# Kernel optimization log

Hardware: AMD Instinct MI355X
Metric: run time of the kernel (lower is better)

## Reference

```python
import jax, jax.numpy as jnp
import numpy as np

D_MODEL = 1024
NUM_HEADS = 16
D_K = D_MODEL // NUM_HEADS
LN_EPS = 1e-5
NEG = -1e9


def setup_inputs() -> dict:
    key = jax.random.key(0)
    ks = jax.random.split(key, 12)
    B, S, D = 8, 1024, D_MODEL
    lim = 1.0 / np.sqrt(D)
    def lin(k):
        k1, k2 = jax.random.split(k)
        W = jax.random.uniform(k1, (D, D), jnp.float32, -lim, lim)
        b = jax.random.uniform(k2, (D,), jnp.float32, -lim, lim)
        return W, b
    Wq, bq = lin(ks[0])
    Wk, bk = lin(ks[1])
    Wv, bv = lin(ks[2])
    Wo, bo = lin(ks[3])
    return {
        "history_items": jax.random.normal(ks[4], (B, S, D), jnp.float32),
        "sequence_mask": jax.random.randint(ks[5], (B, S), 0, 2, jnp.int32),
        "Wq": Wq, "bq": bq, "Wk": Wk, "bk": bk,
        "Wv": Wv, "bv": bv, "Wo": Wo, "bo": bo,
        "ln_gamma": jnp.ones((D,), jnp.float32),
        "ln_beta": jnp.zeros((D,), jnp.float32),
    }


def reference(history_items, sequence_mask, Wq, bq, Wk, bk, Wv, bv, Wo, bo, ln_gamma, ln_beta):
    B, S, D = history_items.shape
    H, dk = NUM_HEADS, D_K
    # projections -> [B, H, S, dk]
    def proj(W, b):
        return (history_items @ W.T + b).reshape(B, S, H, dk).transpose(0, 2, 1, 3)
    q = proj(Wq, bq)
    k = proj(Wk, bk)
    v = proj(Wv, bv)
    # combined mask: causal [1,1,S,S] AND key-padding [B,1,1,S]
    causal = jnp.tril(jnp.ones((S, S), bool))[None, None]
    mask = jnp.logical_and(causal, (sequence_mask != 0)[:, None, None, :])
    scores = jnp.einsum('bhqd,bhkd->bhqk', q, k) / np.sqrt(dk).astype(np.float32)
    scores = jnp.where(mask, scores, NEG)
    attn = jax.nn.softmax(scores, axis=-1)
    ctx = jnp.einsum('bhqk,bhkd->bhqd', attn, v)  # [B,H,S,dk]
    concat = ctx.transpose(0, 2, 1, 3).reshape(B, S, D)
    out = concat @ Wo.T + bo
    x = out + history_items
    mu = jnp.mean(x, axis=-1, keepdims=True)
    var = jnp.mean((x - mu) ** 2, axis=-1, keepdims=True)
    return (x - mu) * jax.lax.rsqrt(var + LN_EPS) * ln_gamma + ln_beta
```

## Files before the change

### kernel.cpp

```cpp
#include <hip/hip_runtime.h>
#include <hip/hip_bf16.h>

#define B_ 8
#define S_ 1024
#define D_ 1024
#define H_ 16
#define DK_ 64
#define M_ (B_*S_)

#define QSCALE 0.1803368801111904f

typedef __attribute__((ext_vector_type(4))) float f32x4;
typedef __attribute__((ext_vector_type(8))) short bf16x8;
typedef __attribute__((ext_vector_type(4))) short s16x4;
typedef __hip_bfloat16 bf16;
typedef unsigned long long ull;

#define GLOAD_LDS16(gp, lp) __builtin_amdgcn_global_load_lds( \
    (const __attribute__((address_space(1))) void*)(gp), \
    (__attribute__((address_space(3))) void*)(lp), 16, 0, 0)

#define SBAR()   asm volatile("s_barrier" ::: "memory")
#define VMCNT(n) asm volatile("s_waitcnt vmcnt(" #n ")" ::: "memory")

__device__ __forceinline__ bf16x8 ld8(const bf16* p){ return *(const bf16x8*)p; }

__device__ __forceinline__ short bf16bits(float f){
  bf16 h = __float2bfloat16(f);
  return __builtin_bit_cast(short, h);
}
__device__ __forceinline__ float tof(short b){
  unsigned u = ((unsigned)(unsigned short)b) << 16;
  return __builtin_bit_cast(float, u);
}
__device__ __forceinline__ int cvtpk(float a, float b){
  int r; asm("v_cvt_pk_bf16_f32 %0, %1, %2" : "=v"(r) : "v"(a), "v"(b)); return r;
}

__device__ __forceinline__ bf16x8 ld8swz(const bf16* base, int row, int colb){
  int sw = colb ^ ((row & 7) << 4);
  return *(const bf16x8*)((const char*)base + row*128 + sw);
}

__global__ __launch_bounds__(256) void cast_all(const float* __restrict__ X,
    const float* __restrict__ w0, const float* __restrict__ w1,
    const float* __restrict__ w2, const float* __restrict__ w3,
    bf16* __restrict__ Xout, bf16* __restrict__ Wout){
  int bid = blockIdx.x;
  if (bid < 4096){
    int i = (bid*256 + threadIdx.x)*8;
    f32x4 a = *(const f32x4*)(X+i);
    f32x4 b = *(const f32x4*)(X+i+4);
    bf16x8 o;
    #pragma unroll
    for (int c=0;c<4;c++){ o[c] = bf16bits(a[c]); o[c+4] = bf16bits(b[c]); }
    *(bf16x8*)(Xout+i) = o;
  } else {
    int bb = bid - 4096;
    int sel = bb >> 9;
    const float* src = (sel==0)?w0:((sel==1)?w1:((sel==2)?w2:w3));
    int i = (((bb & 511)*256) + threadIdx.x)*8;
    f32x4 a = *(const f32x4*)(src+i);
    f32x4 b = *(const f32x4*)(src+i+4);
    bf16x8 o;
    #pragma unroll
    for (int c=0;c<4;c++){ o[c] = bf16bits(a[c]); o[c+4] = bf16bits(b[c]); }
    *(bf16x8*)(Wout + ((size_t)sel<<20) + i) = o;
  }
}

__global__ __launch_bounds__(256) void vmean_kernel(const bf16* __restrict__ Vt_g,
                                                    float* __restrict__ vmean){
  int r = blockIdx.x*4 + (threadIdx.x>>6);
  int lane = threadIdx.x & 63;
  const bf16* p = Vt_g + (((size_t)r)<<10) + lane*16;
  bf16x8 a = ld8(p), c = ld8(p+8);
  float s = 0.f;
  #pragma unroll
  for (int e=0;e<8;e++) s += tof(a[e]) + tof(c[e]);
  #pragma unroll
  for (int off=1;off<64;off<<=1) s += __shfl_xor(s, off);
  if (lane==0) vmean[r] = s * (1.f/1024.f);
}

template<int MODE>
__global__ __launch_bounds__(256) void gemm128(
    const bf16* __restrict__ A,
    const bf16* __restrict__ W0, const bf16* __restrict__ W1, const bf16* __restrict__ W2,
    const float* __restrict__ b0, const float* __restrict__ b1, const float* __restrict__ b2,
    bf16* __restrict__ o0, bf16* __restrict__ o1, bf16* __restrict__ o2,
    const float* __restrict__ resid, float* __restrict__ xout)
{
  const bf16* Wsel = W0; const float* bsel = b0;
  if (MODE==0){
    int z = blockIdx.z;
    Wsel = (z==0)?W0:((z==1)?W1:W2);
    bsel = (z==0)?b0:((z==1)?b1:b2);
  }
  __shared__ bf16 smem[4*128*64];
  const int tid = threadIdx.x, wid = tid>>6, lane = tid&63;
  const int lr = lane&15, lg = lane>>4;
  const int m0 = blockIdx.x*128, n0 = blockIdx.y*128;
  const int wr = wid>>1, wc = wid&1;
  f32x4 acc[4][4] = {};

  auto STAGE = [&](int k0, int bsel_){
    #pragma unroll
    for (int c=0;c<4;c++){
      int ldsoff = ((c<<2)|wid)<<10;
      int off = ldsoff + (lane<<4);
      int row = off>>7;
      int colb = (off&127) ^ ((row&7)<<4);
      GLOAD_LDS16(A   + (((size_t)(m0+row))<<10) + k0 + (colb>>1), (char*)smem + bsel_*32768 + ldsoff);
      GLOAD_LDS16(Wsel+ (((size_t)(n0+row))<<10) + k0 + (colb>>1), (char*)smem + bsel_*32768 + 16384 + ldsoff);
    }
  };

  STAGE(0, 0);
  int cur = 0;
  for (int kt=0; kt<16; kt++){
    if (kt < 15){ STAGE((kt+1)<<6, cur^1); VMCNT(8); }
    else        { VMCNT(0); }
    SBAR();
    __builtin_amdgcn_sched_barrier(0);
    const bf16* Asb = smem + cur*16384;
    const bf16* Bsb = Asb + 8192;
    bf16x8 af[4][2], bfv[4][2];
    #pragma unroll
    for (int m=0;m<4;m++){
      int row = wr*64 + m*16 + lr;
      af[m][0] = ld8swz(Asb, row, lg*16);
      af[m][1] = ld8swz(Asb, row, lg*16 + 64);
    }
    #pragma unroll
    for (int n=0;n<4;n++){
      int row = wc*64 + n*16 + lr;
      bfv[n][0] = ld8swz(Bsb, row, lg*16);
      bfv[n][1] = ld8swz(Bsb, row, lg*16 + 64);
    }
    #pragma unroll
    for (int m=0;m<4;m++)
      #pragma unroll
      for (int n=0;n<4;n++){
        acc[m][n] = __builtin_amdgcn_mfma_f32_16x16x32_bf16(af[m][0], bfv[n][0], acc[m][n],0,0,0);
        acc[m][n] = __builtin_amdgcn_mfma_f32_16x16x32_bf16(af[m][1], bfv[n][1], acc[m][n],0,0,0);
      }
    __builtin_amdgcn_sched_barrier(0);
    SBAR();
    cur ^= 1;
  }

  if (MODE==0){
    if (blockIdx.z == 2){
      __syncthreads();
      #pragma unroll
      for (int n=0;n<4;n++){
        int c = wc*64 + n*16 + lr;
        float bias = bsel[n0 + c];
        #pragma unroll
        for (int m=0;m<4;m++){
          int r0 = wr*64 + m*16 + lg*4;
          s16x4 pk;
          #pragma unroll
          for (int j=0;j<4;j++) pk[j] = bf16bits(acc[m][n][j] + bias);
          *(s16x4*)((char*)smem + c*256 + ((r0*2) ^ ((c&7)<<4))) = pk;
        }
      }
      __syncthreads();
      #pragma unroll
      for (int q=0;q<8;q++){
        int idx = tid + q*256;
        int c = idx>>4, r8 = idx&15;
        bf16x8 vv = *(const bf16x8*)((char*)smem + c*256 + ((r8*16) ^ ((c&7)<<4)));
        int col = n0 + c;  int h = col>>6, dd = col&63;
        int row0 = m0 + r8*8;  int bb = row0>>10, s0 = row0&1023;
        int a = (s0>>3)&3;
        int O = 16*(a&1) + 4*(a>>1);
        bf16* dst = o2 + ((((size_t)bb*H_ + h)*DK_ + dd)<<10) + (s0 & ~31) + O;
        s16x4 lo, hi;
        lo[0]=vv[0]; lo[1]=vv[1]; lo[2]=vv[2]; lo[3]=vv[3];
        hi[0]=vv[4]; hi[1]=vv[5]; hi[2]=vv[6]; hi[3]=vv[7];
        *(s16x4*)dst       = lo;
        *(s16x4*)(dst + 8) = hi;
      }
    } else {
      bf16* osel = (blockIdx.z==0) ? o0 : o1;
      const float qs = (blockIdx.z==0) ? QSCALE : 1.0f;
      #pragma unroll
      for (int n=0;n<4;n++){
        int col = n0 + wc*64 + n*16 + lr;
        float bias = bsel[col];
        int h = col>>6, dd = col&63;
        #pragma unroll
        for (int m=0;m<4;m++)
          #pragma unroll
          for (int j=0;j<4;j++){
            int row = m0 + wr*64 + m*16 + lg*4 + j;
            int bb = row>>10, s = row&1023;
            osel[((((size_t)bb*H_ + h)<<10) + s)*DK_ + dd] = __float2bfloat16((acc[m][n][j] + bias)*qs);
          }
      }
    }
  } else {
    #pragma unroll
    for (int n=0;n<4;n++){
      int col = n0 + wc*64 + n*16 + lr;
      float bias = bsel[col];
      #pragma unroll
      for (int m=0;m<4;m++)
        #pragma unroll
        for (int j=0;j<4;j++){
          int row = m0 + wr*64 + m*16 + lg*4 + j;
          size_t idx = (((size_t)row)<<10) + col;
          xout[idx] = acc[m][n][j] + bias + resid[idx];
        }
    }
  }
}

__global__ __launch_bounds__(512) void attn_kernel(
    const bf16* __restrict__ Q, const bf16* __restrict__ K, const bf16* __restrict__ Vt_g,
    const int* __restrict__ seqm, const float* __restrict__ vmean, bf16* __restrict__ ctxout)
{
  __shared__ bf16 Ks[2][64*64];
  __shared__ bf16 Vs[2][64*64];
  __shared__ int msk[1024];
  const int tid = threadIdx.x, wid = tid>>6, lane = tid&63;
  const int lr = lane&15, lg = lane>>4;
  const int bh = blockIdx.x, xb = blockIdx.y;
  const int b = bh>>4, h = bh&15;
  const bf16* Qb  = Q    + (size_t)bh * S_ * DK_;
  const bf16* Kb  = K    + (size_t)bh * S_ * DK_;
  const bf16* Vtb = Vt_g + (size_t)bh * DK_ * S_;
  for (int i=tid;i<1024;i+=512) msk[i] = seqm[b*1024+i];

  const int g0 = 8*xb + wid;
  const int rb0 = g0*16;
  const int rb1 = (63 - g0)*16;
  bf16x8 qf[2][2];
  {
    const bf16* p0 = Qb + (size_t)(rb0+lr)*DK_ + lg*8;
    const bf16* p1 = Qb + (size_t)(rb1+lr)*DK_ + lg*8;
    qf[0][0] = ld8(p0); qf[0][1] = ld8(p0+32);
    qf[1][0] = ld8(p1); qf[1][1] = ld8(p1+32);
  }
  f32x4 cacc[2][4] = {};
  float lsum[2] = {0.f, 0.f};

  auto STAGE = [&](int t, int bsel){
    const int j0 = t*64;
    int off = (wid<<10) + (lane<<4);
    int row = off>>7;
    int colb = (off&127) ^ ((row&7)<<4);
    GLOAD_LDS16(Kb  + (size_t)(j0+row)*DK_ + (colb>>1), (char*)&Ks[bsel][0] + (wid<<10));
    GLOAD_LDS16(Vtb + (((size_t)row)<<10) + j0 + (colb>>1), (char*)&Vs[bsel][0] + (wid<<10));
  };

  STAGE(0, 0);
  __syncthreads();

  const int bnt = ((1023 - 128*xb) >> 6) + 1;

  int cur = 0;
  for (int t=0; t<bnt; t++){
    VMCNT(0);
    SBAR();
    if (t+1 < bnt) STAGE(t+1, cur^1);
    const int j0 = t*64;
    if (j0 <= rb1 + 15){
      const bool act0 = (j0 <= rb0 + 15);
      ull bt = __ballot(msk[j0 + lane] != 0);
      unsigned btl = (unsigned)bt, bth = (unsigned)(bt >> 32);

      bf16x8 kf[4][2];
      #pragma unroll
      for (int nf=0;nf<4;nf++){
        kf[nf][0] = ld8swz(&Ks[cur][0], nf*16+lr, lg*16);
        kf[nf][1] = ld8swz(&Ks[cur][0], nf*16+lr, lg*16 + 64);
      }

      bf16x8 pf[2][2];
      #pragma unroll
      for (int mf=0;mf<2;mf++){
        if (mf==0 && !act0) continue;
        const int rbm = mf ? rb1 : rb0;
        const bool diag = (j0 + 63 > rbm);
        const int qrel = rbm + lr - j0;
        f32x4 sc[4] = {};
        __builtin_amdgcn_s_setprio(1);
        #pragma unroll
        for (int nf=0;nf<4;nf++){
          sc[nf] = __builtin_amdgcn_mfma_f32_16x16x32_bf16(kf[nf][0], qf[mf][0], sc[nf],0,0,0);
          sc[nf] = __builtin_amdgcn_mfma_f32_16x16x32_bf16(kf[nf][1], qf[mf][1], sc[nf],0,0,0);
        }
        __builtin_amdgcn_s_setprio(0);
        float ls = 0.f;
        #pragma unroll
        for (int nf=0;nf<4;nf++){
          unsigned hb2 = (nf<2) ? btl : bth;
          #pragma unroll
          for (int j=0;j<4;j++){
            float p = exp2f(sc[nf][j]);
            bool ok = ((hb2 >> (16*(nf&1) + 4*lg + j)) & 1u) != 0u;
            if (diag) ok = ok && (16*nf + 4*lg + j <= qrel);
            p = ok ? p : 0.f;
            sc[nf][j] = p;
            ls += p;
          }
        }
        lsum[mf] += ls;
        int4 w0, w1;
        w0.x = cvtpk(sc[0][0], sc[0][1]); w0.y = cvtpk(sc[0][2], sc[0][3]);
        w0.z = cvtpk(sc[1][0], sc[1][1]); w0.w = cvtpk(sc[1][2], sc[1][3]);
        w1.x = cvtpk(sc[2][0], sc[2][1]); w1.y = cvtpk(sc[2][2], sc[2][3]);
        w1.z = cvtpk(sc[3][0], sc[3][1]); w1.w = cvtpk(sc[3][2], sc[3][3]);
        pf[mf][0] = __builtin_bit_cast(bf16x8, w0);
        pf[mf][1] = __builtin_bit_cast(bf16x8, w1);
      }
      __builtin_amdgcn_s_setprio(1);
      #pragma unroll
      for (int df=0;df<4;df++){
        bf16x8 vf0 = ld8swz(&Vs[cur][0], df*16+lr, lg*16);
        bf16x8 vf1 = ld8swz(&Vs[cur][0], df*16+lr, lg*16 + 64);
        if (act0){
          cacc[0][df] = __builtin_amdgcn_mfma_f32_16x16x32_bf16(pf[0][0], vf0, cacc[0][df],0,0,0);
          cacc[0][df] = __builtin_amdgcn_mfma_f32_16x16x32_bf16(pf[0][1], vf1, cacc[0][df],0,0,0);
        }
        cacc[1][df] = __builtin_amdgcn_mfma_f32_16x16x32_bf16(pf[1][0], vf0, cacc[1][df],0,0,0);
        cacc[1][df] = __builtin_amdgcn_mfma_f32_16x16x32_bf16(pf[1][1], vf1, cacc[1][df],0,0,0);
      }
      __builtin_amdgcn_s_setprio(0);
    }
    cur ^= 1;
  }

  #pragma unroll
  for (int mf=0;mf<2;mf++){
    const int rbm = mf ? rb1 : rb0;
    float T = lsum[mf];
    T += __shfl_xor(T, 16);
    T += __shfl_xor(T, 32);
    float lden[4];
    #pragma unroll
    for (int j=0;j<4;j++)
      lden[j] = __shfl(T, (lane & 48) | (lg*4 + j));
    #pragma unroll
    for (int df=0;df<4;df++)
      #pragma unroll
      for (int j=0;j<4;j++){
        int srow = rbm + lg*4 + j;
        int dd = df*16 + lr;
        float v = cacc[mf][df][j] / lden[j];
        if (lden[j] < 1e-30f) v = vmean[bh*64 + dd];
        ctxout[((size_t)b*S_ + srow)*D_ + h*DK_ + dd] = __float2bfloat16(v);
      }
  }
}

__global__ __launch_bounds__(256) void ln_kernel(const float* __restrict__ X2,
    const float* __restrict__ gamma, const float* __restrict__ beta, float* __restrict__ out)
{
  const int row = blockIdx.x, tid = threadIdx.x;
  const int lane = tid&63, wid = tid>>6;
  const f32x4* xr = (const f32x4*)(X2 + (((size_t)row)<<10));
  f32x4 v = xr[tid];
  float s  = v[0]+v[1]+v[2]+v[3];
  float s2 = v[0]*v[0]+v[1]*v[1]+v[2]*v[2]+v[3]*v[3];
  #pragma unroll
  for (int off=1;off<64;off<<=1){ s += __shfl_xor(s,off); s2 += __shfl_xor(s2,off); }
  __shared__ float red[8];
  if (lane==0){ red[wid]=s; red[wid+4]=s2; }
  __syncthreads();
  s  = red[0]+red[1]+red[2]+red[3];
  s2 = red[4]+red[5]+red[6]+red[7];
  float mu  = s*(1.f/1024.f);
  float var = s2*(1.f/1024.f) - mu*mu;
  float inv = rsqrtf(var + 1e-5f);
  f32x4 gv = ((const f32x4*)gamma)[tid], bv = ((const f32x4*)beta)[tid];
  f32x4 o;
  #pragma unroll
  for (int c=0;c<4;c++) o[c] = (v[c]-mu)*inv*gv[c] + bv[c];
  ((f32x4*)(out + (((size_t)row)<<10)))[tid] = o;
}

extern "C" void kernel_launch(void* const* d_in, const int* in_sizes, int n_in,
                              void* d_out, int out_size, void* d_ws, size_t ws_size,
                              hipStream_t stream) {
  const float* X   = (const float*)d_in[0];
  const int*   sm  = (const int*)d_in[1];
  const float* Wq  = (const float*)d_in[2];  const float* bq = (const float*)d_in[3];
  const float* Wk  = (const float*)d_in[4];  const float* bk = (const float*)d_in[5];
  const float* Wv  = (const float*)d_in[6];  const float* bv = (const float*)d_in[7];
  const float* Wo  = (const float*)d_in[8];  const float* bo = (const float*)d_in[9];
  const float* ga  = (const float*)d_in[10]; const float* be = (const float*)d_in[11];
  float* out = (float*)d_out;
  char* ws = (char*)d_ws;

  bf16* Xbf = (bf16*)(ws);
  bf16* Wqb = (bf16*)(ws + (16u<<20));
  bf16* Wkb = (bf16*)(ws + (18u<<20));
  bf16* Wvb = (bf16*)(ws + (20u<<20));
  bf16* Wob = (bf16*)(ws + (22u<<20));
  bf16* Qh  = (bf16*)(ws + (24u<<20));
  bf16* Kh  = (bf16*)(ws + (40u<<20));
  bf16* Vth = (bf16*)(ws + (56u<<20));
  bf16* Ctx = (bf16*)(ws + (72u<<20));
  float* X2 = (float*)(ws + (24u<<20));
  float* vmean = (float*)(ws + (16u<<20));

  cast_all<<<6144,256,0,stream>>>(X, Wq, Wk, Wv, Wo, Xbf, Wqb);

  dim3 g1(M_/128, D_/128, 3);
  gemm128<0><<<g1,256,0,stream>>>(Xbf, Wqb,Wkb,Wvb, bq,bk,bv, Qh,Kh,Vth, nullptr, nullptr);

  vmean_kernel<<<B_*H_*DK_/4,256,0,stream>>>(Vth, vmean);

  dim3 g2(B_*H_, 4);
  attn_kernel<<<g2,512,0,stream>>>(Qh, Kh, Vth, sm, vmean, Ctx);

  dim3 g3(M_/128, D_/128, 1);
  gemm128<1><<<g3,256,0,stream>>>(Ctx, Wob,nullptr,nullptr, bo,nullptr,nullptr,
                                  nullptr,nullptr,nullptr, X, X2);

  ln_kernel<<<M_,256,0,stream>>>(X2, ga, be, out);
}
```

Measured before the change: 184.0 us.

## Transpose MFMA operands for vectorized epilogue stores and store residual sum as bf16

Swaps the MFMA operand order in the Q/K and output-projection GEMMs so each lane holds four consecutive columns. Bias loads, residual loads and output stores can then be done as 4-wide vectors instead of scalar strided accesses. The V projection moves to its own kernel instantiation that keeps the original LDS-transpose epilogue. The post-projection residual sum is now stored in bf16 instead of fp32, halving write and read traffic for the layernorm input. The cost is an extra kernel launch and reduced precision on the pre-layernorm activations.

```diff
diff --git a/kernel.cpp b/kernel.cpp
--- a/kernel.cpp
+++ b/kernel.cpp
@@ -86,17 +86,13 @@
 template<int MODE>
 __global__ __launch_bounds__(256) void gemm128(
     const bf16* __restrict__ A,
-    const bf16* __restrict__ W0, const bf16* __restrict__ W1, const bf16* __restrict__ W2,
-    const float* __restrict__ b0, const float* __restrict__ b1, const float* __restrict__ b2,
-    bf16* __restrict__ o0, bf16* __restrict__ o1, bf16* __restrict__ o2,
-    const float* __restrict__ resid, float* __restrict__ xout)
+    const bf16* __restrict__ W0, const bf16* __restrict__ W1,
+    const float* __restrict__ b0, const float* __restrict__ b1,
+    bf16* __restrict__ o0, bf16* __restrict__ o1,
+    const float* __restrict__ resid)
 {
   const bf16* Wsel = W0; const float* bsel = b0;
-  if (MODE==0){
-    int z = blockIdx.z;
-    Wsel = (z==0)?W0:((z==1)?W1:W2);
-    bsel = (z==0)?b0:((z==1)?b1:b2);
-  }
+  if (MODE==0 && blockIdx.z == 1){ Wsel = W1; bsel = b1; }
   __shared__ bf16 smem[4*128*64];
   const int tid = threadIdx.x, wid = tid>>6, lane = tid&63;
   const int lr = lane&15, lg = lane>>4;
@@ -142,8 +138,13 @@
     for (int m=0;m<4;m++)
       #pragma unroll
       for (int n=0;n<4;n++){
-        acc[m][n] = __builtin_amdgcn_mfma_f32_16x16x32_bf16(af[m][0], bfv[n][0], acc[m][n],0,0,0);
-        acc[m][n] = __builtin_amdgcn_mfma_f32_16x16x32_bf16(af[m][1], bfv[n][1], acc[m][n],0,0,0);
+        if (MODE==2){
+          acc[m][n] = __builtin_amdgcn_mfma_f32_16x16x32_bf16(af[m][0], bfv[n][0], acc[m][n],0,0,0);
+          acc[m][n] = __builtin_amdgcn_mfma_f32_16x16x32_bf16(af[m][1], bfv[n][1], acc[m][n],0,0,0);
+        } else {
+          acc[m][n] = __builtin_amdgcn_mfma_f32_16x16x32_bf16(bfv[n][0], af[m][0], acc[m][n],0,0,0);
+          acc[m][n] = __builtin_amdgcn_mfma_f32_16x16x32_bf16(bfv[n][1], af[m][1], acc[m][n],0,0,0);
+        }
       }
     __builtin_amdgcn_sched_barrier(0);
     SBAR();
@@ -151,69 +152,69 @@
   }
 
   if (MODE==0){
-    if (blockIdx.z == 2){
-      __syncthreads();
+    bf16* osel = (blockIdx.z==0) ? o0 : o1;
+    const float qs = (blockIdx.z==0) ? QSCALE : 1.0f;
+    #pragma unroll
+    for (int m=0;m<4;m++){
+      int row_tok = m0 + wr*64 + m*16 + lr;
+      int bb = row_tok>>10, ss = row_tok&1023;
       #pragma unroll
       for (int n=0;n<4;n++){
-        int c = wc*64 + n*16 + lr;
-        float bias = bsel[n0 + c];
+        int col0 = n0 + wc*64 + n*16 + lg*4;
+        int h = col0>>6, dd0 = col0&63;
+        f32x4 bias4 = *(const f32x4*)(bsel + col0);
+        s16x4 pk;
         #pragma unroll
-        for (int m=0;m<4;m++){
-          int r0 = wr*64 + m*16 + lg*4;
-          s16x4 pk;
-          #pragma unroll
-          for (int j=0;j<4;j++) pk[j] = bf16bits(acc[m][n][j] + bias);
-          *(s16x4*)((char*)smem + c*256 + ((r0*2) ^ ((c&7)<<4))) = pk;
-        }
-      }
-      __syncthreads();
-      #pragma unroll
-      for (int q=0;q<8;q++){
-        int idx = tid + q*256;
-        int c = idx>>4, r8 = idx&15;
-        bf16x8 vv = *(const bf16x8*)((char*)smem + c*256 + ((r8*16) ^ ((c&7)<<4)));
-        int col = n0 + c;  int h = col>>6, dd = col&63;
-        int row0 = m0 + r8*8;  int bb = row0>>10, s0 = row0&1023;
-        int a = (s0>>3)&3;
-        int O = 16*(a&1) + 4*(a>>1);
-        bf16* dst = o2 + ((((size_t)bb*H_ + h)*DK_ + dd)<<10) + (s0 & ~31) + O;
-        s16x4 lo, hi;
-        lo[0]=vv[0]; lo[1]=vv[1]; lo[2]=vv[2]; lo[3]=vv[3];
-        hi[0]=vv[4]; hi[1]=vv[5]; hi[2]=vv[6]; hi[3]=vv[7];
-        *(s16x4*)dst       = lo;
-        *(s16x4*)(dst + 8) = hi;
-      }
-    } else {
-      bf16* osel = (blockIdx.z==0) ? o0 : o1;
-      const float qs = (blockIdx.z==0) ? QSCALE : 1.0f;
+        for (int j=0;j<4;j++) pk[j] = bf16bits((acc[m][n][j] + bias4[j])*qs);
+        *(s16x4*)(osel + ((((size_t)bb*H_ + h)<<10) + ss)*DK_ + dd0) = pk;
+      }
+    }
+  } else if (MODE==1){
+    #pragma unroll
+    for (int m=0;m<4;m++){
+      int row_tok = m0 + wr*64 + m*16 + lr;
       #pragma unroll
       for (int n=0;n<4;n++){
-        int col = n0 + wc*64 + n*16 + lr;
-        float bias = bsel[col];
-        int h = col>>6, dd = col&63;
+        int col0 = n0 + wc*64 + n*16 + lg*4;
+        f32x4 bias4 = *(const f32x4*)(b0 + col0);
+        f32x4 rv = *(const f32x4*)(resid + (((size_t)row_tok)<<10) + col0);
+        s16x4 pk;
         #pragma unroll
-        for (int m=0;m<4;m++)
-          #pragma unroll
-          for (int j=0;j<4;j++){
-            int row = m0 + wr*64 + m*16 + lg*4 + j;
-            int bb = row>>10, s = row&1023;
-            osel[((((size_t)bb*H_ + h)<<10) + s)*DK_ + dd] = __float2bfloat16((acc[m][n][j] + bias)*qs);
-          }
+        for (int j=0;j<4;j++) pk[j] = bf16bits(acc[m][n][j] + bias4[j] + rv[j]);
+        *(s16x4*)(o0 + (((size_t)row_tok)<<10) + col0) = pk;
       }
     }
   } else {
+    __syncthreads();
     #pragma unroll
     for (int n=0;n<4;n++){
-      int col = n0 + wc*64 + n*16 + lr;
-      float bias = bsel[col];
-      #pragma unroll
-      for (int m=0;m<4;m++)
+      int c = wc*64 + n*16 + lr;
+      float bias = b0[n0 + c];
+      #pragma unroll
+      for (int m=0;m<4;m++){
+        int r0 = wr*64 + m*16 + lg*4;
+        s16x4 pk;
         #pragma unroll
-        for (int j=0;j<4;j++){
-          int row = m0 + wr*64 + m*16 + lg*4 + j;
-          size_t idx = (((size_t)row)<<10) + col;
-          xout[idx] = acc[m][n][j] + bias + resid[idx];
-        }
+        for (int j=0;j<4;j++) pk[j] = bf16bits(acc[m][n][j] + bias);
+        *(s16x4*)((char*)smem + c*256 + ((r0*2) ^ ((c&7)<<4))) = pk;
+      }
+    }
+    __syncthreads();
+    #pragma unroll
+    for (int q=0;q<8;q++){
+      int idx = tid + q*256;
+      int c = idx>>4, r8 = idx&15;
+      bf16x8 vv = *(const bf16x8*)((char*)smem + c*256 + ((r8*16) ^ ((c&7)<<4)));
+      int col = n0 + c;  int h = col>>6, dd = col&63;
+      int row0 = m0 + r8*8;  int bb = row0>>10, s0 = row0&1023;
+      int a = (s0>>3)&3;
+      int O = 16*(a&1) + 4*(a>>1);
+      bf16* dst = o0 + ((((size_t)bb*H_ + h)*DK_ + dd)<<10) + (s0 & ~31) + O;
+      s16x4 lo, hi;
+      lo[0]=vv[0]; lo[1]=vv[1]; lo[2]=vv[2]; lo[3]=vv[3];
+      hi[0]=vv[4]; hi[1]=vv[5]; hi[2]=vv[6]; hi[3]=vv[7];
+      *(s16x4*)dst       = lo;
+      *(s16x4*)(dst + 8) = hi;
     }
   }
 }
@@ -357,13 +358,16 @@
   }
 }
 
-__global__ __launch_bounds__(256) void ln_kernel(const float* __restrict__ X2,
+__global__ __launch_bounds__(256) void ln_kernel(const bf16* __restrict__ X2,
     const float* __restrict__ gamma, const float* __restrict__ beta, float* __restrict__ out)
 {
   const int row = blockIdx.x, tid = threadIdx.x;
   const int lane = tid&63, wid = tid>>6;
-  const f32x4* xr = (const f32x4*)(X2 + (((size_t)row)<<10));
-  f32x4 v = xr[tid];
+  const s16x4* xr = (const s16x4*)(X2 + (((size_t)row)<<10));
+  s16x4 xv = xr[tid];
+  f32x4 v;
+  #pragma unroll
+  for (int c=0;c<4;c++) v[c] = tof(xv[c]);
   float s  = v[0]+v[1]+v[2]+v[3];
   float s2 = v[0]*v[0]+v[1]*v[1]+v[2]*v[2]+v[3]*v[3];
   #pragma unroll
@@ -405,13 +409,15 @@
   bf16* Kh  = (bf16*)(ws + (40u<<20));
   bf16* Vth = (bf16*)(ws + (56u<<20));
   bf16* Ctx = (bf16*)(ws + (72u<<20));
-  float* X2 = (float*)(ws + (24u<<20));
+  bf16* X2b = (bf16*)(ws + (24u<<20));
   float* vmean = (float*)(ws + (16u<<20));
 
   cast_all<<<6144,256,0,stream>>>(X, Wq, Wk, Wv, Wo, Xbf, Wqb);
 
-  dim3 g1(M_/128, D_/128, 3);
-  gemm128<0><<<g1,256,0,stream>>>(Xbf, Wqb,Wkb,Wvb, bq,bk,bv, Qh,Kh,Vth, nullptr, nullptr);
+  dim3 g1(M_/128, D_/128, 2);
+  gemm128<0><<<g1,256,0,stream>>>(Xbf, Wqb, Wkb, bq, bk, Qh, Kh, nullptr);
+  dim3 g1v(M_/128, D_/128, 1);
+  gemm128<2><<<g1v,256,0,stream>>>(Xbf, Wvb, nullptr, bv, nullptr, Vth, nullptr, nullptr);
 
   vmean_kernel<<<B_*H_*DK_/4,256,0,stream>>>(Vth, vmean);
 
@@ -419,8 +425,7 @@
   attn_kernel<<<g2,512,0,stream>>>(Qh, Kh, Vth, sm, vmean, Ctx);
 
   dim3 g3(M_/128, D_/128, 1);
-  gemm128<1><<<g3,256,0,stream>>>(Ctx, Wob,nullptr,nullptr, bo,nullptr,nullptr,
-                                  nullptr,nullptr,nullptr, X, X2);
-
-  ln_kernel<<<M_,256,0,stream>>>(X2, ga, be, out);
-}
+  gemm128<1><<<g3,256,0,stream>>>(Ctx, Wob, nullptr, bo, nullptr, X2b, nullptr, X);
+
+  ln_kernel<<<M_,256,0,stream>>>(X2b, ga, be, out);
+}
```

New measurement: 190.8 us. 1.04x slower.
